# Performance work log

Measured on AMD Instinct MI355X. Metric: run time of the kernel, lower is better.

## Reference

```python
import jax, jax.numpy as jnp
import numpy as np

G = 256      # num graphs
M = 256      # max nodes per graph
N = G * M    # total nodes
E = N * 16   # total edges
C = 3        # num_class
K = 5        # prototypes per class
D = 128      # embedding_dim
MAXLEN = 3   # max_length


def setup_inputs() -> dict:
    key = jax.random.key(0)
    ks = jax.random.split(key, 8)
    hg = jax.random.normal(ks[0], (G, D), jnp.float32)
    H_init = jax.random.normal(ks[1], (C, K, D), jnp.float32)
    path_weight = jnp.ones((MAXLEN,), jnp.float32) * 0.5
    # per-class edge attention in (0,1), strictly interior for infoloss logs
    sij = jax.random.uniform(ks[2], (C, E), jnp.float32) * 0.98 + 0.01
    # edges constrained within each graph (batch is block-contiguous)
    src = jax.random.randint(ks[3], (E,), 0, N)
    dst = (src // M) * M + jax.random.randint(ks[4], (E,), 0, M)
    edge_index = jnp.stack([src, dst]).astype(jnp.int32)
    batch = (jnp.arange(N) // M).astype(jnp.int32)
    s = jax.random.randint(ks[5], (G,), 0, M).astype(jnp.int32)
    t = jax.random.randint(ks[6], (G,), 0, M).astype(jnp.int32)
    return dict(hg=hg, H_init=H_init, path_weight=path_weight, sij=sij,
                edge_index=edge_index, batch=batch, s=s, t=t)


def check_zero(x):
    return jnp.where(x == 0, x + 1e-8, x)


def to_dense_adj(edge_index, batch, vals):
    # scatter edge vals into [G, M, M] dense per-graph adjacency
    src, dst = edge_index[0], edge_index[1]
    g = batch[src]
    r = src - g * M
    c = dst - g * M
    return jnp.zeros((G, M, M), vals.dtype).at[g, r, c].add(vals)


def infoloss(att):
    r = 0.5
    return (att * jnp.log(att / r + 1e-6)
            + (1 - att) * jnp.log((1 - att) / (1 - r + 1e-6) + 1e-6)).mean()


def path_loss3(Mdj, Adj, s, t, weight):
    gid = jnp.arange(G)
    u = Mdj[gid, s, :]            # [G, M]
    mk = Mdj[gid, :, t]           # [G, M]
    a = Adj[gid, s, :]
    ak = Adj[gid, :, t]
    uk = Mdj[gid, s, t] / check_zero(Adj[gid, s, t])
    for l in range(MAXLEN - 1):
        tmp = (u * mk) / check_zero(a * ak)
        w = jnp.power(tmp.max(axis=1) + 1e-8, jnp.float32(1.0 / (l + 1)))
        uk = uk + weight[l + 1] * w
        # power iteration: u <- u @ Mdj, a <- a @ Adj (batched over graphs)
        u = jnp.einsum('gm,gmn->gn', u, Mdj)
        a = jnp.einsum('gm,gmn->gn', a, Adj)
    uk = uk / MAXLEN
    return -jnp.mean(jnp.log(uk + 1e-8))


def reference(hg, H_init, path_weight, sij, edge_index, batch, s, t):
    # binary dense adjacency (detached in original)
    Adj = jax.lax.stop_gradient(
        to_dense_adj(edge_index, batch, jnp.ones((E,), jnp.float32)))
    weight = jnp.clip(path_weight, 1e-10, 1.0)

    def per_class(Hc, sij_c):
        # per-class prototype attention
        scores = hg @ Hc.T                     # [G, K]
        att = jax.nn.softmax(scores, axis=-1)
        H_emb = att @ Hc                       # [G, D]
        # dense weighted adjacency from per-class edge attention
        Mdj = to_dense_adj(edge_index, batch, sij_c)
        L_path = path_loss3(Mdj, Adj, s, t, weight)
        L_l2 = (jnp.sum(sij_c ** 2) / 2) / G
        L_info = infoloss(sij_c)
        return H_emb, L_info, L_path, L_l2

    H_out, L_info, L_path, L_l2 = jax.vmap(per_class)(H_init, sij)
    return (H_out, L_info.mean(), L_path.mean(), L_l2.mean())
```

## Files before the change

kernel.cpp:

```cpp
#include <hip/hip_runtime.h>
#include <math.h>

#define G 256
#define M 256
#define NNODES (G*M)
#define EDGES (NNODES*16)
#define C 3
#define K 5
#define D 128
#define GM (G*M)

#define OFF_U0   0
#define OFF_MK0  196608
#define OFF_U1   393216
#define OFF_A0   589824
#define OFF_AK0  655360
#define OFF_A1   720896
#define OFF_MST  786432
#define OFF_AST  787200
#define ZERO_FLOATS 787456
#define NB_A     1024
#define OFF_PINFO 787456
#define OFF_PL2   (OFF_PINFO + NB_A)
#define OFF_PPATH (OFF_PL2 + NB_A)
#define WS_FLOATS (OFF_PPATH + C*G)

__device__ __forceinline__ float waveReduceSum(float v) {
    #pragma unroll
    for (int o = 32; o > 0; o >>= 1) v += __shfl_xor(v, o, 64);
    return v;
}
__device__ __forceinline__ float waveReduceMax(float v) {
    #pragma unroll
    for (int o = 32; o > 0; o >>= 1) v = fmaxf(v, __shfl_xor(v, o, 64));
    return v;
}

__global__ void passA(const float* __restrict__ sij, const int* __restrict__ ei,
                      const int* __restrict__ s, const int* __restrict__ t,
                      float* __restrict__ ws) {
    float* u0  = ws + OFF_U0;
    float* mk0 = ws + OFF_MK0;
    float* a0  = ws + OFF_A0;
    float* ak0 = ws + OFF_AK0;
    float* Mst = ws + OFF_MST;
    float* Ast = ws + OFF_AST;

    float info = 0.f, l2 = 0.f;
    for (int e = blockIdx.x * blockDim.x + threadIdx.x; e < EDGES;
         e += NB_A * 256) {
        int src = ei[e], dst = ei[EDGES + e];
        int g = src >> 8;
        int r = src & 255;
        int c = dst - (g << 8);
        int sg = s[g], tg = t[g];
        bool isr = (r == sg), isc = (c == tg);
        float v[C];
        #pragma unroll
        for (int cc = 0; cc < C; ++cc) v[cc] = sij[cc * EDGES + e];
        if (isr) {
            #pragma unroll
            for (int cc = 0; cc < C; ++cc) atomicAdd(&u0[cc * GM + (g << 8) + c], v[cc]);
            atomicAdd(&a0[(g << 8) + c], 1.0f);
        }
        if (isc) {
            #pragma unroll
            for (int cc = 0; cc < C; ++cc) atomicAdd(&mk0[cc * GM + (g << 8) + r], v[cc]);
            atomicAdd(&ak0[(g << 8) + r], 1.0f);
        }
        if (isr && isc) {
            #pragma unroll
            for (int cc = 0; cc < C; ++cc) atomicAdd(&Mst[cc * G + g], v[cc]);
            atomicAdd(&Ast[g], 1.0f);
        }
        #pragma unroll
        for (int cc = 0; cc < C; ++cc) {
            float x = v[cc];
            info += x * logf(x * 2.0f + 1e-6f)
                  + (1.0f - x) * logf((1.0f - x) / 0.500001f + 1e-6f);
            l2 += x * x;
        }
    }
    info = waveReduceSum(info);
    l2 = waveReduceSum(l2);
    __shared__ float sInfo[4], sL2[4];
    int wid = threadIdx.x >> 6, lane = threadIdx.x & 63;
    if (lane == 0) { sInfo[wid] = info; sL2[wid] = l2; }
    __syncthreads();
    if (threadIdx.x == 0) {
        float i2 = 0.f, l = 0.f;
        #pragma unroll
        for (int w = 0; w < 4; ++w) { i2 += sInfo[w]; l += sL2[w]; }
        ws[OFF_PINFO + blockIdx.x] = i2;
        ws[OFF_PL2 + blockIdx.x] = l;
    }
}

__global__ void passB(const float* __restrict__ sij, const int* __restrict__ ei,
                      float* __restrict__ ws) {
    int e = blockIdx.x * blockDim.x + threadIdx.x;
    if (e >= EDGES) return;
    const float* u0 = ws + OFF_U0;
    const float* a0 = ws + OFF_A0;
    float* u1 = ws + OFF_U1;
    float* a1 = ws + OFF_A1;
    int src = ei[e], dst = ei[EDGES + e];
    int g = src >> 8;
    int r = src & 255;
    int c = dst - (g << 8);
    float ar = a0[(g << 8) + r];
    if (ar == 0.0f) return;
    atomicAdd(&a1[(g << 8) + c], ar);
    #pragma unroll
    for (int cc = 0; cc < C; ++cc) {
        float ur = u0[cc * GM + (g << 8) + r];
        atomicAdd(&u1[cc * GM + (g << 8) + c], ur * sij[cc * EDGES + e]);
    }
}

__global__ void embK(const float* __restrict__ hg, const float* __restrict__ H,
                     float* __restrict__ out) {
    int b = blockIdx.x;
    int c = b / G, g = b - c * G;
    int d = threadIdx.x;
    float h = hg[g * D + d];
    __shared__ float sc[K];
    __shared__ float att[K];
    if (threadIdx.x < K) sc[threadIdx.x] = 0.f;
    __syncthreads();
    #pragma unroll
    for (int k = 0; k < K; ++k) {
        float p = h * H[(c * K + k) * D + d];
        p = waveReduceSum(p);
        if ((threadIdx.x & 63) == 0) atomicAdd(&sc[k], p);
    }
    __syncthreads();
    if (threadIdx.x == 0) {
        float m = sc[0];
        #pragma unroll
        for (int k = 1; k < K; ++k) m = fmaxf(m, sc[k]);
        float sum = 0.f, ex[K];
        #pragma unroll
        for (int k = 0; k < K; ++k) { ex[k] = expf(sc[k] - m); sum += ex[k]; }
        #pragma unroll
        for (int k = 0; k < K; ++k) att[k] = ex[k] / sum;
    }
    __syncthreads();
    float o = 0.f;
    #pragma unroll
    for (int k = 0; k < K; ++k) o += att[k] * H[(c * K + k) * D + d];
    out[(c * G + g) * D + d] = o;
}

__global__ void pathK(const float* __restrict__ pw, float* __restrict__ ws) {
    int b = blockIdx.x;
    int c = b / G, g = b - c * G;
    int x = threadIdx.x;
    const float* u0  = ws + OFF_U0;
    const float* mk0 = ws + OFF_MK0;
    const float* u1  = ws + OFF_U1;
    const float* a0  = ws + OFF_A0;
    const float* ak0 = ws + OFF_AK0;
    const float* a1  = ws + OFF_A1;
    const float* Mst = ws + OFF_MST;
    const float* Ast = ws + OFF_AST;

    int gi  = (g << 8) + x;
    int cgi = c * GM + gi;
    float ak = ak0[gi], mk = mk0[cgi];
    float den0 = a0[gi] * ak;  den0 = (den0 == 0.f) ? 1e-8f : den0;
    float t0 = u0[cgi] * mk / den0;
    float den1 = a1[gi] * ak;  den1 = (den1 == 0.f) ? 1e-8f : den1;
    float t1 = u1[cgi] * mk / den1;

    t0 = waveReduceMax(t0);
    t1 = waveReduceMax(t1);
    __shared__ float s0[4], s1[4];
    int wid = threadIdx.x >> 6, lane = threadIdx.x & 63;
    if (lane == 0) { s0[wid] = t0; s1[wid] = t1; }
    __syncthreads();
    if (threadIdx.x == 0) {
        float m0 = s0[0], m1 = s1[0];
        #pragma unroll
        for (int w = 1; w < 4; ++w) { m0 = fmaxf(m0, s0[w]); m1 = fmaxf(m1, s1[w]); }
        float w1 = fminf(fmaxf(pw[1], 1e-10f), 1.0f);
        float w2 = fminf(fmaxf(pw[2], 1e-10f), 1.0f);
        float A = Ast[g];  A = (A == 0.f) ? 1e-8f : A;
        float uk = Mst[c * G + g] / A;
        uk += w1 * (m0 + 1e-8f);
        uk += w2 * sqrtf(m1 + 1e-8f);
        uk *= (1.0f / 3.0f);
        ws[OFF_PPATH + b] = logf(uk + 1e-8f);
    }
}

__global__ void finalK(const float* __restrict__ ws, float* __restrict__ out) {
    int tid = threadIdx.x;
    float info = 0.f, l2 = 0.f, path = 0.f;
    for (int i = tid; i < NB_A; i += 256) {
        info += ws[OFF_PINFO + i];
        l2   += ws[OFF_PL2 + i];
    }
    for (int i = tid; i < C * G; i += 256) path += ws[OFF_PPATH + i];
    info = waveReduceSum(info);
    l2   = waveReduceSum(l2);
    path = waveReduceSum(path);
    __shared__ float sI[4], sL[4], sP[4];
    int wid = tid >> 6, lane = tid & 63;
    if (lane == 0) { sI[wid] = info; sL[wid] = l2; sP[wid] = path; }
    __syncthreads();
    if (tid == 0) {
        float i2 = 0.f, l = 0.f, p = 0.f;
        #pragma unroll
        for (int w = 0; w < 4; ++w) { i2 += sI[w]; l += sL[w]; p += sP[w]; }
        out[C * G * D + 0] = i2 / (float)(C * EDGES);
        out[C * G * D + 1] = -p / (float)(C * G);
        out[C * G * D + 2] = l / (2.0f * (float)G * (float)C);
    }
}

extern "C" void kernel_launch(void* const* d_in, const int* in_sizes, int n_in,
                              void* d_out, int out_size, void* d_ws, size_t ws_size,
                              hipStream_t stream) {
    const float* hg  = (const float*)d_in[0];
    const float* H   = (const float*)d_in[1];
    const float* pw  = (const float*)d_in[2];
    const float* sij = (const float*)d_in[3];
    const int*   ei  = (const int*)d_in[4];
    const int*   s   = (const int*)d_in[6];
    const int*   t   = (const int*)d_in[7];
    float* out = (float*)d_out;
    float* ws  = (float*)d_ws;

    hipMemsetAsync(d_ws, 0, ZERO_FLOATS * sizeof(float), stream);
    passA<<<NB_A, 256, 0, stream>>>(sij, ei, s, t, ws);
    passB<<<EDGES / 256, 256, 0, stream>>>(sij, ei, ws);
    embK<<<C * G, D, 0, stream>>>(hg, H, out);
    pathK<<<C * G, M, 0, stream>>>(pw, ws);
    finalK<<<1, 256, 0, stream>>>(ws, out);
}
```

Measured before the change: 45.89 us.

## Fuse embedding into edge pass, vectorize edge loads, use fast log

Prototype-attention embedding blocks are appended to the edge-processing launch, which removes one kernel launch. Edge indices and attention values are now loaded as int4/float4, with four edges per thread in both edge passes. The grid-stride loop is dropped in favour of a fixed 1024-block grid covering all edges. logf is replaced by __logf, which cuts transcendental cost at some accuracy risk.

```diff
diff --git a/kernel.cpp b/kernel.cpp
--- a/kernel.cpp
+++ b/kernel.cpp
@@ -19,10 +19,11 @@
 #define OFF_MST  786432
 #define OFF_AST  787200
 #define ZERO_FLOATS 787456
-#define NB_A     1024
+#define NB_EDGE  1024
+#define NB_EMB   384
 #define OFF_PINFO 787456
-#define OFF_PL2   (OFF_PINFO + NB_A)
-#define OFF_PPATH (OFF_PL2 + NB_A)
+#define OFF_PL2   (OFF_PINFO + NB_EDGE)
+#define OFF_PPATH (OFF_PL2 + NB_EDGE)
 #define WS_FLOATS (OFF_PPATH + C*G)
 
 __device__ __forceinline__ float waveReduceSum(float v) {
@@ -38,7 +39,45 @@
 
 __global__ void passA(const float* __restrict__ sij, const int* __restrict__ ei,
                       const int* __restrict__ s, const int* __restrict__ t,
-                      float* __restrict__ ws) {
+                      const float* __restrict__ hg, const float* __restrict__ H,
+                      float* __restrict__ out, float* __restrict__ ws) {
+    __shared__ float sc[2][K];
+    __shared__ float att[2][K];
+    __shared__ float sInfo[4], sL2[4];
+
+    if (blockIdx.x >= NB_EDGE) {
+        int half = threadIdx.x >> 7;
+        int d = threadIdx.x & 127;
+        int pair = (blockIdx.x - NB_EDGE) * 2 + half;
+        int c = pair / G, g = pair - c * G;
+        float h = hg[g * D + d];
+        if (d < K) sc[half][d] = 0.f;
+        __syncthreads();
+        #pragma unroll
+        for (int k = 0; k < K; ++k) {
+            float p = h * H[(c * K + k) * D + d];
+            p = waveReduceSum(p);
+            if ((threadIdx.x & 63) == 0) atomicAdd(&sc[half][k], p);
+        }
+        __syncthreads();
+        if (d == 0) {
+            float m = sc[half][0];
+            #pragma unroll
+            for (int k = 1; k < K; ++k) m = fmaxf(m, sc[half][k]);
+            float sum = 0.f, ex[K];
+            #pragma unroll
+            for (int k = 0; k < K; ++k) { ex[k] = expf(sc[half][k] - m); sum += ex[k]; }
+            #pragma unroll
+            for (int k = 0; k < K; ++k) att[half][k] = ex[k] / sum;
+        }
+        __syncthreads();
+        float o = 0.f;
+        #pragma unroll
+        for (int k = 0; k < K; ++k) o += att[half][k] * H[(c * K + k) * D + d];
+        out[pair * D + d] = o;
+        return;
+    }
+
     float* u0  = ws + OFF_U0;
     float* mk0 = ws + OFF_MK0;
     float* a0  = ws + OFF_A0;
@@ -46,44 +85,54 @@
     float* Mst = ws + OFF_MST;
     float* Ast = ws + OFF_AST;
 
+    int tid = blockIdx.x * 256 + threadIdx.x;
+    int e0 = tid * 4;
+    int4 src4 = *(const int4*)(ei + e0);
+    int4 dst4 = *(const int4*)(ei + EDGES + e0);
+    float4 v0 = *(const float4*)(sij + 0 * EDGES + e0);
+    float4 v1 = *(const float4*)(sij + 1 * EDGES + e0);
+    float4 v2 = *(const float4*)(sij + 2 * EDGES + e0);
+
+    const int* srcp = (const int*)&src4;
+    const int* dstp = (const int*)&dst4;
+    const float* v0p = (const float*)&v0;
+    const float* v1p = (const float*)&v1;
+    const float* v2p = (const float*)&v2;
+
     float info = 0.f, l2 = 0.f;
-    for (int e = blockIdx.x * blockDim.x + threadIdx.x; e < EDGES;
-         e += NB_A * 256) {
-        int src = ei[e], dst = ei[EDGES + e];
+    #pragma unroll
+    for (int j = 0; j < 4; ++j) {
+        int src = srcp[j], dst = dstp[j];
         int g = src >> 8;
         int r = src & 255;
         int c = dst - (g << 8);
         int sg = s[g], tg = t[g];
-        bool isr = (r == sg), isc = (c == tg);
-        float v[C];
-        #pragma unroll
-        for (int cc = 0; cc < C; ++cc) v[cc] = sij[cc * EDGES + e];
-        if (isr) {
+        float v[C] = { v0p[j], v1p[j], v2p[j] };
+        if (r == sg) {
             #pragma unroll
             for (int cc = 0; cc < C; ++cc) atomicAdd(&u0[cc * GM + (g << 8) + c], v[cc]);
             atomicAdd(&a0[(g << 8) + c], 1.0f);
-        }
-        if (isc) {
+            if (c == tg) {
+                #pragma unroll
+                for (int cc = 0; cc < C; ++cc) atomicAdd(&Mst[cc * G + g], v[cc]);
+                atomicAdd(&Ast[g], 1.0f);
+            }
+        }
+        if (c == tg) {
             #pragma unroll
             for (int cc = 0; cc < C; ++cc) atomicAdd(&mk0[cc * GM + (g << 8) + r], v[cc]);
             atomicAdd(&ak0[(g << 8) + r], 1.0f);
         }
-        if (isr && isc) {
-            #pragma unroll
-            for (int cc = 0; cc < C; ++cc) atomicAdd(&Mst[cc * G + g], v[cc]);
-            atomicAdd(&Ast[g], 1.0f);
-        }
         #pragma unroll
         for (int cc = 0; cc < C; ++cc) {
             float x = v[cc];
-            info += x * logf(x * 2.0f + 1e-6f)
-                  + (1.0f - x) * logf((1.0f - x) / 0.500001f + 1e-6f);
+            info += x * __logf(x * 2.0f + 1e-6f)
+                  + (1.0f - x) * __logf((1.0f - x) / 0.500001f + 1e-6f);
             l2 += x * x;
         }
     }
     info = waveReduceSum(info);
     l2 = waveReduceSum(l2);
-    __shared__ float sInfo[4], sL2[4];
     int wid = threadIdx.x >> 6, lane = threadIdx.x & 63;
     if (lane == 0) { sInfo[wid] = info; sL2[wid] = l2; }
     __syncthreads();
@@ -98,58 +147,34 @@
 
 __global__ void passB(const float* __restrict__ sij, const int* __restrict__ ei,
                       float* __restrict__ ws) {
-    int e = blockIdx.x * blockDim.x + threadIdx.x;
-    if (e >= EDGES) return;
     const float* u0 = ws + OFF_U0;
     const float* a0 = ws + OFF_A0;
     float* u1 = ws + OFF_U1;
     float* a1 = ws + OFF_A1;
-    int src = ei[e], dst = ei[EDGES + e];
-    int g = src >> 8;
-    int r = src & 255;
-    int c = dst - (g << 8);
-    float ar = a0[(g << 8) + r];
-    if (ar == 0.0f) return;
-    atomicAdd(&a1[(g << 8) + c], ar);
-    #pragma unroll
-    for (int cc = 0; cc < C; ++cc) {
-        float ur = u0[cc * GM + (g << 8) + r];
-        atomicAdd(&u1[cc * GM + (g << 8) + c], ur * sij[cc * EDGES + e]);
-    }
-}
-
-__global__ void embK(const float* __restrict__ hg, const float* __restrict__ H,
-                     float* __restrict__ out) {
-    int b = blockIdx.x;
-    int c = b / G, g = b - c * G;
-    int d = threadIdx.x;
-    float h = hg[g * D + d];
-    __shared__ float sc[K];
-    __shared__ float att[K];
-    if (threadIdx.x < K) sc[threadIdx.x] = 0.f;
-    __syncthreads();
-    #pragma unroll
-    for (int k = 0; k < K; ++k) {
-        float p = h * H[(c * K + k) * D + d];
-        p = waveReduceSum(p);
-        if ((threadIdx.x & 63) == 0) atomicAdd(&sc[k], p);
-    }
-    __syncthreads();
-    if (threadIdx.x == 0) {
-        float m = sc[0];
-        #pragma unroll
-        for (int k = 1; k < K; ++k) m = fmaxf(m, sc[k]);
-        float sum = 0.f, ex[K];
-        #pragma unroll
-        for (int k = 0; k < K; ++k) { ex[k] = expf(sc[k] - m); sum += ex[k]; }
-        #pragma unroll
-        for (int k = 0; k < K; ++k) att[k] = ex[k] / sum;
-    }
-    __syncthreads();
-    float o = 0.f;
-    #pragma unroll
-    for (int k = 0; k < K; ++k) o += att[k] * H[(c * K + k) * D + d];
-    out[(c * G + g) * D + d] = o;
+
+    int tid = blockIdx.x * 256 + threadIdx.x;
+    int e0 = tid * 4;
+    int4 src4 = *(const int4*)(ei + e0);
+    int4 dst4 = *(const int4*)(ei + EDGES + e0);
+    const int* srcp = (const int*)&src4;
+    const int* dstp = (const int*)&dst4;
+
+    #pragma unroll
+    for (int j = 0; j < 4; ++j) {
+        int src = srcp[j], dst = dstp[j];
+        int g = src >> 8;
+        int r = src & 255;
+        int c = dst - (g << 8);
+        float ar = a0[(g << 8) + r];
+        if (ar == 0.0f) continue;
+        atomicAdd(&a1[(g << 8) + c], ar);
+        int e = e0 + j;
+        #pragma unroll
+        for (int cc = 0; cc < C; ++cc) {
+            float ur = u0[cc * GM + (g << 8) + r];
+            atomicAdd(&u1[cc * GM + (g << 8) + c], ur * sij[cc * EDGES + e]);
+        }
+    }
 }
 
 __global__ void pathK(const float* __restrict__ pw, float* __restrict__ ws) {
@@ -190,14 +215,14 @@
         uk += w1 * (m0 + 1e-8f);
         uk += w2 * sqrtf(m1 + 1e-8f);
         uk *= (1.0f / 3.0f);
-        ws[OFF_PPATH + b] = logf(uk + 1e-8f);
+        ws[OFF_PPATH + b] = __logf(uk + 1e-8f);
     }
 }
 
 __global__ void finalK(const float* __restrict__ ws, float* __restrict__ out) {
     int tid = threadIdx.x;
     float info = 0.f, l2 = 0.f, path = 0.f;
-    for (int i = tid; i < NB_A; i += 256) {
+    for (int i = tid; i < NB_EDGE; i += 256) {
         info += ws[OFF_PINFO + i];
         l2   += ws[OFF_PL2 + i];
     }
@@ -233,9 +258,8 @@
     float* ws  = (float*)d_ws;
 
     hipMemsetAsync(d_ws, 0, ZERO_FLOATS * sizeof(float), stream);
-    passA<<<NB_A, 256, 0, stream>>>(sij, ei, s, t, ws);
-    passB<<<EDGES / 256, 256, 0, stream>>>(sij, ei, ws);
-    embK<<<C * G, D, 0, stream>>>(hg, H, out);
+    passA<<<NB_EDGE + NB_EMB, 256, 0, stream>>>(sij, ei, s, t, hg, H, out, ws);
+    passB<<<NB_EDGE, 256, 0, stream>>>(sij, ei, ws);
     pathK<<<C * G, M, 0, stream>>>(pw, ws);
     finalK<<<1, 256, 0, stream>>>(ws, out);
 }
```

After: 42.51 us. -7.4%, faster.
